# Performance work log

Hardware: AMD Instinct MI355X
Metric: run time of the kernel (lower is better)

## Reference

```python
import jax, jax.numpy as jnp
import numpy as np

B, LA, LS, C, H = 4, 1536, 512, 256, 4
DK = C // H
NEG = -jnp.inf


def _pad(lengths, maxlen):
    # True where padded (idx >= length)
    return jnp.arange(maxlen)[None, :] >= lengths[:, None]


def build_mask(l_v, l_s, ilens, ylens):
    """Additive float mask [B, l_v+l_s, l_v+l_s] with 0 / -inf, matching
    generate_multi_modal_mask_new."""
    b = ilens.shape[0]
    i = jnp.arange(l_s)
    causal = jnp.where(i[:, None] >= i[None, :], 0.0, NEG)            # [l_s, l_s]
    tgt_pad = _pad(ylens, l_s)                                        # [b, l_s]
    mask_s_s = jnp.where(tgt_pad[:, None, :], NEG, causal[None])      # [b, l_s, l_s]
    src_row = jnp.where(_pad(ilens, l_v), NEG, 0.0)                   # [b, l_v]
    mask_v_v = jnp.broadcast_to(src_row[:, None, :], (b, l_v, l_v))
    mask_s_v = jnp.broadcast_to(src_row[:, None, :], (b, l_s, l_v))
    mask_v_s = jnp.full((b, l_v, l_s), NEG, dtype=jnp.float32)
    top = jnp.concatenate([mask_v_v, mask_v_s], axis=2)
    bot = jnp.concatenate([mask_s_v, mask_s_s], axis=2)
    return jnp.concatenate([top, bot], axis=1)


def setup_inputs() -> dict:
    key = jax.random.key(0)
    ks = jax.random.split(key, 12)
    scale = 1.0 / np.sqrt(C)
    return {
        "audio_encoder_out": jax.random.normal(ks[0], (B, LA, C), jnp.float32),
        "text_encoder_out": jax.random.normal(ks[1], (B, LS, C), jnp.float32),
        "speech_length": jax.random.randint(ks[2], (B,), 1, LA),
        "text_length": jax.random.randint(ks[3], (B,), 1, LS),
        "Wq": jax.random.normal(ks[4], (C, C), jnp.float32) * scale,
        "bq": jax.random.normal(ks[5], (C,), jnp.float32) * scale,
        "Wk": jax.random.normal(ks[6], (C, C), jnp.float32) * scale,
        "bk": jax.random.normal(ks[7], (C,), jnp.float32) * scale,
        "Wv": jax.random.normal(ks[8], (C, C), jnp.float32) * scale,
        "bv": jax.random.normal(ks[9], (C,), jnp.float32) * scale,
        "Wo": jax.random.normal(ks[10], (C, C), jnp.float32) * scale,
        "bo": jax.random.normal(ks[11], (C,), jnp.float32) * scale,
    }


def reference(audio_encoder_out, text_encoder_out, speech_length, text_length,
              Wq, bq, Wk, bk, Wv, bv, Wo, bo):
    b, l_a, c = audio_encoder_out.shape
    l_s = text_encoder_out.shape[1]
    x = jnp.concatenate([audio_encoder_out, text_encoder_out], axis=1)  # [B, L, C]
    L = l_a + l_s

    def heads(W, bias):
        return (x @ W.T + bias).reshape(b, L, H, DK).transpose(0, 2, 1, 3)  # [B,H,L,DK]

    q, k, v = heads(Wq, bq), heads(Wk, bk), heads(Wv, bv)
    scores = jnp.einsum("bhqd,bhkd->bhqk", q, k) / np.float32(np.sqrt(DK))

    amask = build_mask(l_a, l_s, speech_length, text_length)  # additive [B,L,L]
    # Faithful to torch: mask.eq(0) positions (additive-0) are filled with -inf,
    # then zeroed in attn (the module's inverted masking behavior).
    eq0 = (amask == 0.0)[:, None, :, :]                       # [B,1,L,L]
    scores = jnp.where(eq0, NEG, scores)
    attn = jax.nn.softmax(scores, axis=-1)
    attn = jnp.where(eq0, 0.0, attn)                          # (dropout = identity, eval)
    out = jnp.einsum("bhqk,bhkd->bhqd", attn, v)
    out = out.transpose(0, 2, 1, 3).reshape(b, L, H * DK)
    return out @ Wo.T + bo
```

## Files before the change

### kernel.cpp

```cpp
#include <hip/hip_runtime.h>
#include <hip/hip_bf16.h>
#include <math.h>

#define LA 1536
#define LS 512
#define LT 2048
#define CC 256
#define NH 4
#define DKH 64
#define NB 4
#define NT (LT / 64)
#define NTA (LA / 64)

typedef _Float16 f16;
typedef __attribute__((ext_vector_type(8))) _Float16 f16x8;
typedef __attribute__((ext_vector_type(4))) _Float16 f16x4;
typedef __attribute__((ext_vector_type(4))) float f32x4;

__device__ inline f16x8 cvt8(const float4 a, const float4 b) {
    f16x8 h;
    h[0] = (_Float16)a.x; h[1] = (_Float16)a.y; h[2] = (_Float16)a.z; h[3] = (_Float16)a.w;
    h[4] = (_Float16)b.x; h[5] = (_Float16)b.y; h[6] = (_Float16)b.z; h[7] = (_Float16)b.w;
    return h;
}

__global__ __launch_bounds__(256) void qkv_mfma(
    const float* __restrict__ audio, const float* __restrict__ text,
    const float* __restrict__ Wq, const float* __restrict__ bq,
    const float* __restrict__ Wk, const float* __restrict__ bk,
    const float* __restrict__ Wv, const float* __restrict__ bv,
    f16* __restrict__ Qh, f16* __restrict__ Kh, f16* __restrict__ Vth)
{
    __shared__ f16 smem[128 * 64 + 64 * 64];
    f16* As = smem;
    f16* Bs = smem + 128 * 64;

    const int tid = threadIdx.x;
    const int w = tid >> 6, l = tid & 63;
    const int g = l >> 4, r = l & 15;

    const int m0 = blockIdx.x * 128;
    const int n0 = blockIdx.y * 64;
    const int mat = n0 >> 8;
    const int ch0 = n0 & 255;

    const float* W    = (mat == 0) ? Wq : (mat == 1) ? Wk : Wv;
    const float* bias = (mat == 0) ? bq : (mat == 1) ? bk : bv;

    const int b  = m0 >> 11;
    const int l0 = m0 & 2047;

    f32x4 acc[2][4] = {};

    for (int k0 = 0; k0 < CC; k0 += 64) {
        #pragma unroll
        for (int m = 0; m < 4; ++m) {
            const int idx = m * 256 + tid;
            const int row = idx >> 3, c = idx & 7;
            const int lrow = l0 + row;
            const float* src = (lrow < LA)
                ? (audio + ((size_t)b * LA + lrow) * CC + k0 + c * 8)
                : (text  + ((size_t)b * LS + (lrow - LA)) * CC + k0 + c * 8);
            const float4 x0 = *(const float4*)src;
            const float4 x1 = *(const float4*)(src + 4);
            *(f16x8*)(As + row * 64 + ((c ^ (row & 7)) << 3)) = cvt8(x0, x1);
        }
        #pragma unroll
        for (int m = 0; m < 2; ++m) {
            const int idx = m * 256 + tid;
            const int row = idx >> 3, c = idx & 7;
            const float* src = W + (size_t)(ch0 + row) * CC + k0 + c * 8;
            const float4 x0 = *(const float4*)src;
            const float4 x1 = *(const float4*)(src + 4);
            *(f16x8*)(Bs + row * 64 + ((c ^ (row & 7)) << 3)) = cvt8(x0, x1);
        }
        __syncthreads();
        #pragma unroll
        for (int kc = 0; kc < 2; ++kc) {
            f16x8 af[2];
            #pragma unroll
            for (int i = 0; i < 2; ++i) {
                const int row = w * 32 + i * 16 + r;
                const int c = kc * 4 + g;
                af[i] = *(const f16x8*)(As + row * 64 + ((c ^ (row & 7)) << 3));
            }
            f16x8 bf[4];
            #pragma unroll
            for (int j = 0; j < 4; ++j) {
                const int row = j * 16 + r;
                const int c = kc * 4 + g;
                bf[j] = *(const f16x8*)(Bs + row * 64 + ((c ^ (row & 7)) << 3));
            }
            #pragma unroll
            for (int i = 0; i < 2; ++i)
                #pragma unroll
                for (int j = 0; j < 4; ++j)
                    acc[i][j] = __builtin_amdgcn_mfma_f32_16x16x32_f16(af[i], bf[j], acc[i][j], 0, 0, 0);
        }
        __syncthreads();
    }

    float bcol[4];
    #pragma unroll
    for (int j = 0; j < 4; ++j) bcol[j] = bias[ch0 + j * 16 + r];

    if (mat <= 1) {
        f16* Out = (mat == 0) ? Qh : Kh;
        #pragma unroll
        for (int i = 0; i < 2; ++i)
            #pragma unroll
            for (int e = 0; e < 4; ++e) {
                const int m = m0 + w * 32 + i * 16 + g * 4 + e;
                #pragma unroll
                for (int j = 0; j < 4; ++j)
                    Out[(size_t)m * CC + ch0 + j * 16 + r] = (_Float16)(acc[i][j][e] + bcol[j]);
            }
    } else {
        f16* Ts = smem;
        #pragma unroll
        for (int i = 0; i < 2; ++i)
            #pragma unroll
            for (int e = 0; e < 4; ++e) {
                const int ml = w * 32 + i * 16 + g * 4 + e;
                #pragma unroll
                for (int j = 0; j < 4; ++j)
                    Ts[(j * 16 + r) * 136 + ml] = (_Float16)(acc[i][j][e] + bcol[j]);
            }
        __syncthreads();
        const int b2 = m0 >> 11, l0m = m0 & 2047;
        #pragma unroll
        for (int u = 0; u < 4; ++u) {
            const int idx = u * 256 + tid;
            const int nl = idx >> 4, mc = idx & 15;
            const f16x8 vv = *(const f16x8*)(Ts + nl * 136 + mc * 8);
            const int nglob = ch0 + nl;
            const int hh = nglob >> 6, dd = nglob & 63;
            *(f16x8*)(Vth + ((size_t)((b2 * NH + hh) * DKH + dd)) * LT + l0m + mc * 8) = vv;
        }
    }
}

__global__ __launch_bounds__(512) void attn_f16(
    const f16* __restrict__ Q, const f16* __restrict__ K,
    const f16* __restrict__ Vt,
    const int* __restrict__ slen, const int* __restrict__ tlen,
    f16* __restrict__ AO)
{
    __shared__ f16 Ks[2][4096];
    __shared__ f16 Vts[2][4096];
    __shared__ f16 Ps[8][16 * 72];
    __shared__ float Oc[4][1024];
    __shared__ float ML[2][64][2];

    const int tid = threadIdx.x;
    const int w = tid >> 6, l = tid & 63;
    const int gid = w >> 2, wg = w & 3;
    const int g = l >> 4, r = l & 15;
    const int tg = tid & 255;

    const int q0 = blockIdx.x * 64;
    const int h  = blockIdx.y;
    const int b  = blockIdx.z;

    const int ilen = slen[b];
    const int kcap = LA + tlen[b];
    const int nskip = ilen >> 6;
    int ntskip = 0;
    if (q0 >= LA) {
        const int skipmax = min(q0 - 63, kcap - 64);
        const int d = skipmax - LA;
        ntskip = (d < 0) ? 0 : ((d >> 6) + 1);
    }
    const int nAudio = NTA - nskip;
    const int nProc  = nAudio + (NT - NTA) - ntskip;
    const int nIter  = (nProc + 1) >> 1;

    const int qrow = q0 + 16 * wg + r;

    f16x8 qf[2];
    #pragma unroll
    for (int ch = 0; ch < 2; ++ch) {
        f16x8 q8 = *(const f16x8*)(Q + ((size_t)(b * LT) + qrow) * CC + h * DKH + ch * 32 + g * 8);
        #pragma unroll
        for (int e = 0; e < 8; ++e) q8[e] = q8[e] * (_Float16)0.125f;
        qf[ch] = q8;
    }

    const int srow0 = tg >> 3, scc = tg & 7;
    const int srow1 = srow0 + 32;
    const int sdst0 = srow0 * 64 + ((scc ^ (srow0 & 7)) << 3);
    const int sdst1 = srow1 * 64 + ((scc ^ (srow1 & 7)) << 3);

    #define TILE_OF(p) ((p) < nAudio ? (nskip + (p)) : (NTA + ntskip + ((p) - nAudio)))

    {
        const int k0 = TILE_OF(gid) * 64;
        *(f16x8*)(Ks[gid] + sdst0)  = *(const f16x8*)(K  + ((size_t)(b * LT) + k0 + srow0) * CC + h * DKH + scc * 8);
        *(f16x8*)(Vts[gid] + sdst0) = *(const f16x8*)(Vt + ((size_t)((b * NH + h) * DKH) + srow0) * LT + k0 + scc * 8);
        *(f16x8*)(Ks[gid] + sdst1)  = *(const f16x8*)(K  + ((size_t)(b * LT) + k0 + srow1) * CC + h * DKH + scc * 8);
        *(f16x8*)(Vts[gid] + sdst1) = *(const f16x8*)(Vt + ((size_t)((b * NH + h) * DKH) + srow1) * LT + k0 + scc * 8);
    }

    float m_run = -1e30f, l_run = 0.0f;
    f32x4 o[4] = {};

    for (int i = 0; i < nIter; ++i) {
        __syncthreads();
        const int pcur = 2 * i + gid;
        const bool curV = pcur < nProc;
        const bool nxtV = (pcur + 2) < nProc;

        f16x8 kr0, vr0, kr1, vr1;
        if (nxtV) {
            const int kn = TILE_OF(pcur + 2) * 64;
            kr0 = *(const f16x8*)(K  + ((size_t)(b * LT) + kn + srow0) * CC + h * DKH + scc * 8);
            vr0 = *(const f16x8*)(Vt + ((size_t)((b * NH + h) * DKH) + srow0) * LT + kn + scc * 8);
            kr1 = *(const f16x8*)(K  + ((size_t)(b * LT) + kn + srow1) * CC + h * DKH + scc * 8);
            vr1 = *(const f16x8*)(Vt + ((size_t)((b * NH + h) * DKH) + srow1) * LT + kn + scc * 8);
        }

        if (curV) {
            const int kt = TILE_OF(pcur);
            const int k0 = kt * 64;

            f32x4 sacc[4] = {};
            #pragma unroll
            for (int s = 0; s < 4; ++s) {
                const int row = 16 * s + r;
                #pragma unroll
                for (int ch = 0; ch < 2; ++ch) {
                    const f16x8 a = *(const f16x8*)(Ks[gid] + row * 64 + ((((ch * 4 + g) ^ (row & 7)) & 7) << 3));
                    sacc[s] = __builtin_amdgcn_mfma_f32_16x16x32_f16(a, qf[ch], sacc[s], 0, 0, 0);
                }
            }

            const int mode = (kt < NTA) ? ((k0 >= ilen) ? 0 : 1)
                                        : ((q0 < LA) ? 0 : 2);
            float sv[16];
            if (mode == 0) {
                #pragma unroll
                for (int s = 0; s < 4; ++s)
                    #pragma unroll
                    for (int e = 0; e < 4; ++e) sv[s * 4 + e] = sacc[s][e];
            } else if (mode == 1) {
                #pragma unroll
                for (int s = 0; s < 4; ++s)
                    #pragma unroll
                    for (int e = 0; e < 4; ++e) {
                        const int kk = k0 + 16 * s + 4 * g + e;
                        sv[s * 4 + e] = (kk >= ilen) ? sacc[s][e] : -INFINITY;
                    }
            } else {
                #pragma unroll
                for (int s = 0; s < 4; ++s)
                    #pragma unroll
                    for (int e = 0; e < 4; ++e) {
                        const int kk = k0 + 16 * s + 4 * g + e;
                        sv[s * 4 + e] = (kk > qrow || kk >= kcap) ? sacc[s][e] : -INFINITY;
                    }
            }

            float mloc = -1e30f;
            #pragma unroll
            for (int u = 0; u < 16; ++u) mloc = fmaxf(mloc, sv[u]);
            mloc = fmaxf(mloc, __shfl_xor(mloc, 16));
            mloc = fmaxf(mloc, __shfl_xor(mloc, 32));
            const float m_new = fmaxf(m_run, mloc);

            float ssum = 0.0f;
            f16x4 ph[4];
            #pragma unroll
            for (int s = 0; s < 4; ++s)
                #pragma unroll
                for (int e = 0; e < 4; ++e) {
                    const float p = __expf(sv[s * 4 + e] - m_new);
                    ph[s][e] = (_Float16)p;
                    ssum += p;
                }
            ssum += __shfl_xor(ssum, 16);
            ssum += __shfl_xor(ssum, 32);
            const float sc = __expf(m_run - m_new);
            l_run = l_run * sc + ssum;
            m_run = m_new;

            #pragma unroll
            for (int s = 0; s < 4; ++s)
                *(f16x4*)(&Ps[w][0] + r * 72 + 16 * s + 4 * g) = ph[s];

            #pragma unroll
            for (int e = 0; e < 4; ++e) {
                const float scr = __shfl(sc, 4 * g + e);
                #pragma unroll
                for (int dsb = 0; dsb < 4; ++dsb) o[dsb][e] *= scr;
            }

            #pragma unroll
            for (int ch = 0; ch < 2; ++ch) {
                const f16x8 a = *(const f16x8*)(&Ps[w][0] + r * 72 + ch * 32 + g * 8);
                #pragma unroll
                for (int dsb = 0; dsb < 4; ++dsb) {
                    const int vrow = 16 * dsb + r;
                    const f16x8 bf = *(const f16x8*)(Vts[gid] + vrow * 64 + ((((ch * 4 + g) ^ (vrow & 7)) & 7) << 3));
                    o[dsb] = __builtin_amdgcn_mfma_f32_16x16x32_f16(a, bf, o[dsb], 0, 0, 0);
                }
            }
        }

        __syncthreads();
        if (nxtV) {
            *(f16x8*)(Ks[gid] + sdst0)  = kr0;
            *(f16x8*)(Vts[gid] + sdst0) = vr0;
            *(f16x8*)(Ks[gid] + sdst1)  = kr1;
            *(f16x8*)(Vts[gid] + sdst1) = vr1;
        }
    }

    if (g == 0) {
        ML[gid][16 * wg + r][0] = m_run;
        ML[gid][16 * wg + r][1] = l_run;
    }
    if (gid == 1) {
        #pragma unroll
        for (int dsb = 0; dsb < 4; ++dsb)
            *(f32x4*)&Oc[wg][dsb * 256 + (g * 16 + r) * 4] = o[dsb];
    }
    __syncthreads();

    if (gid == 0) {
        #pragma unroll
        for (int e = 0; e < 4; ++e) {
            const int qloc = 16 * wg + 4 * g + e;
            const float m0v = ML[0][qloc][0], l0v = ML[0][qloc][1];
            const float m1v = ML[1][qloc][0], l1v = ML[1][qloc][1];
            const float mt = fmaxf(m0v, m1v);
            const float c0 = __expf(m0v - mt);
            const float c1 = __expf(m1v - mt);
            const float inv = 1.0f / (l0v * c0 + l1v * c1);
            const int qq = q0 + qloc;
            #pragma unroll
            for (int dsb = 0; dsb < 4; ++dsb) {
                const float of = (o[dsb][e] * c0 + Oc[wg][dsb * 256 + (g * 16 + r) * 4 + e] * c1) * inv;
                AO[((size_t)(b * LT) + qq) * CC + h * DKH + 16 * dsb + r] = (_Float16)of;
            }
        }
    }
    #undef TILE_OF
}

__global__ __launch_bounds__(256) void out_mfma(
    const f16* __restrict__ X, const float* __restrict__ Wo,
    const float* __restrict__ bo, float* __restrict__ Out)
{
    __shared__ f16 As[128 * 64];
    __shared__ f16 Bs[64 * 64];

    const int tid = threadIdx.x;
    const int w = tid >> 6, l = tid & 63;
    const int g = l >> 4, r = l & 15;

    const int m0 = blockIdx.x * 128;
    const int n0 = blockIdx.y * 64;

    f32x4 acc[2][4] = {};

    for (int k0 = 0; k0 < CC; k0 += 64) {
        #pragma unroll
        for (int m = 0; m < 4; ++m) {
            const int idx = m * 256 + tid;
            const int row = idx >> 3, c = idx & 7;
            *(f16x8*)(As + row * 64 + ((c ^ (row & 7)) << 3)) =
                *(const f16x8*)(X + (size_t)(m0 + row) * CC + k0 + c * 8);
        }
        #pragma unroll
        for (int m = 0; m < 2; ++m) {
            const int idx = m * 256 + tid;
            const int row = idx >> 3, c = idx & 7;
            const float* src = Wo + (size_t)(n0 + row) * CC + k0 + c * 8;
            const float4 x0 = *(const float4*)src;
            const float4 x1 = *(const float4*)(src + 4);
            *(f16x8*)(Bs + row * 64 + ((c ^ (row & 7)) << 3)) = cvt8(x0, x1);
        }
        __syncthreads();
        #pragma unroll
        for (int kc = 0; kc < 2; ++kc) {
            f16x8 af[2];
            #pragma unroll
            for (int i = 0; i < 2; ++i) {
                const int row = w * 32 + i * 16 + r;
                const int c = kc * 4 + g;
                af[i] = *(const f16x8*)(As + row * 64 + ((c ^ (row & 7)) << 3));
            }
            f16x8 bf[4];
            #pragma unroll
            for (int j = 0; j < 4; ++j) {
                const int row = j * 16 + r;
                const int c = kc * 4 + g;
                bf[j] = *(const f16x8*)(Bs + row * 64 + ((c ^ (row & 7)) << 3));
            }
            #pragma unroll
            for (int i = 0; i < 2; ++i)
                #pragma unroll
                for (int j = 0; j < 4; ++j)
                    acc[i][j] = __builtin_amdgcn_mfma_f32_16x16x32_f16(af[i], bf[j], acc[i][j], 0, 0, 0);
        }
        __syncthreads();
    }

    float bcol[4];
    #pragma unroll
    for (int j = 0; j < 4; ++j) bcol[j] = bo[n0 + j * 16 + r];

    #pragma unroll
    for (int i = 0; i < 2; ++i)
        #pragma unroll
        for (int e = 0; e < 4; ++e) {
            const int m = m0 + w * 32 + i * 16 + g * 4 + e;
            #pragma unroll
            for (int j = 0; j < 4; ++j)
                Out[(size_t)m * CC + n0 + j * 16 + r] = acc[i][j][e] + bcol[j];
        }
}

extern "C" void kernel_launch(void* const* d_in, const int* in_sizes, int n_in,
                              void* d_out, int out_size, void* d_ws, size_t ws_size,
                              hipStream_t stream)
{
    const float* audio = (const float*)d_in[0];
    const float* text  = (const float*)d_in[1];
    const int*   slen  = (const int*)d_in[2];
    const int*   tlen  = (const int*)d_in[3];
    const float* Wq = (const float*)d_in[4];
    const float* bq = (const float*)d_in[5];
    const float* Wk = (const float*)d_in[6];
    const float* bk = (const float*)d_in[7];
    const float* Wv = (const float*)d_in[8];
    const float* bv = (const float*)d_in[9];
    const float* Wo = (const float*)d_in[10];
    const float* bo = (const float*)d_in[11];
    float* out = (float*)d_out;

    const size_t SZ = (size_t)NB * LT * CC;
    f16* Qh  = (f16*)d_ws;
    f16* Kh  = Qh + SZ;
    f16* Vth = Kh + SZ;
    f16* AOh = Vth + SZ;

    qkv_mfma<<<dim3(64, 12), 256, 0, stream>>>(audio, text, Wq, bq, Wk, bk, Wv, bv,
                                               Qh, Kh, Vth);
    attn_f16<<<dim3(LT / 64, NH, NB), 512, 0, stream>>>(Qh, Kh, Vth, slen, tlen, AOh);
    out_mfma<<<dim3(64, 4), 256, 0, stream>>>(AOh, Wo, bo, out);
}
```

Baseline: 49.30 us.

## Split attention KV range four ways with combine kernel, widen GEMM tiles

Attention now uses a flash-decoding style split: each block handles every fourth KV tile and writes normalized partial outputs plus per-row max/sum, and a new combine kernel merges them. The aim is more blocks in flight and shorter per-block loops. The Q scale and log2(e) are folded into the QKV epilogue so the softmax can use exp2f, and rescaling of the running output is skipped when the running max is unchanged. The QKV and output GEMMs move to 128-wide N tiles, giving fewer blocks with more reuse. This adds a kernel launch and extra workspace traffic for the partial outputs.

```diff
diff --git a/kernel.cpp b/kernel.cpp
--- a/kernel.cpp
+++ b/kernel.cpp
@@ -11,6 +11,10 @@
 #define NB 4
 #define NT (LT / 64)
 #define NTA (LA / 64)
+#define NSPLIT 4
+#define SZ ((size_t)NB * LT * CC)
+
+#define QSCALE 0.1803368801111244f
 
 typedef _Float16 f16;
 typedef __attribute__((ext_vector_type(8))) _Float16 f16x8;
@@ -31,7 +35,7 @@
     const float* __restrict__ Wv, const float* __restrict__ bv,
     f16* __restrict__ Qh, f16* __restrict__ Kh, f16* __restrict__ Vth)
 {
-    __shared__ f16 smem[128 * 64 + 64 * 64];
+    __shared__ f16 smem[128 * 64 + 128 * 64];
     f16* As = smem;
     f16* Bs = smem + 128 * 64;
 
@@ -40,9 +44,9 @@
     const int g = l >> 4, r = l & 15;
 
     const int m0 = blockIdx.x * 128;
-    const int n0 = blockIdx.y * 64;
-    const int mat = n0 >> 8;
-    const int ch0 = n0 & 255;
+    const int n0g = blockIdx.y * 128;
+    const int mat = n0g >> 8;
+    const int ch0 = n0g & 255;
 
     const float* W    = (mat == 0) ? Wq : (mat == 1) ? Wk : Wv;
     const float* bias = (mat == 0) ? bq : (mat == 1) ? bk : bv;
@@ -50,12 +54,12 @@
     const int b  = m0 >> 11;
     const int l0 = m0 & 2047;
 
-    f32x4 acc[2][4] = {};
+    f32x4 acc[2][8] = {};
 
     for (int k0 = 0; k0 < CC; k0 += 64) {
         #pragma unroll
-        for (int m = 0; m < 4; ++m) {
-            const int idx = m * 256 + tid;
+        for (int mm = 0; mm < 4; ++mm) {
+            const int idx = mm * 256 + tid;
             const int row = idx >> 3, c = idx & 7;
             const int lrow = l0 + row;
             const float* src = (lrow < LA)
@@ -66,8 +70,8 @@
             *(f16x8*)(As + row * 64 + ((c ^ (row & 7)) << 3)) = cvt8(x0, x1);
         }
         #pragma unroll
-        for (int m = 0; m < 2; ++m) {
-            const int idx = m * 256 + tid;
+        for (int mm = 0; mm < 4; ++mm) {
+            const int idx = mm * 256 + tid;
             const int row = idx >> 3, c = idx & 7;
             const float* src = W + (size_t)(ch0 + row) * CC + k0 + c * 8;
             const float4 x0 = *(const float4*)src;
@@ -84,83 +88,91 @@
                 const int c = kc * 4 + g;
                 af[i] = *(const f16x8*)(As + row * 64 + ((c ^ (row & 7)) << 3));
             }
-            f16x8 bf[4];
-            #pragma unroll
-            for (int j = 0; j < 4; ++j) {
-                const int row = j * 16 + r;
-                const int c = kc * 4 + g;
-                bf[j] = *(const f16x8*)(Bs + row * 64 + ((c ^ (row & 7)) << 3));
-            }
-            #pragma unroll
-            for (int i = 0; i < 2; ++i)
-                #pragma unroll
-                for (int j = 0; j < 4; ++j)
-                    acc[i][j] = __builtin_amdgcn_mfma_f32_16x16x32_f16(af[i], bf[j], acc[i][j], 0, 0, 0);
-        }
-        __syncthreads();
-    }
-
-    float bcol[4];
-    #pragma unroll
-    for (int j = 0; j < 4; ++j) bcol[j] = bias[ch0 + j * 16 + r];
+            #pragma unroll
+            for (int jh = 0; jh < 2; ++jh) {
+                f16x8 bf[4];
+                #pragma unroll
+                for (int j = 0; j < 4; ++j) {
+                    const int row = (jh * 4 + j) * 16 + r;
+                    const int c = kc * 4 + g;
+                    bf[j] = *(const f16x8*)(Bs + row * 64 + ((c ^ (row & 7)) << 3));
+                }
+                #pragma unroll
+                for (int i = 0; i < 2; ++i)
+                    #pragma unroll
+                    for (int j = 0; j < 4; ++j)
+                        acc[i][jh * 4 + j] = __builtin_amdgcn_mfma_f32_16x16x32_f16(
+                            af[i], bf[j], acc[i][jh * 4 + j], 0, 0, 0);
+            }
+        }
+        __syncthreads();
+    }
+
+    float bcol[8];
+    #pragma unroll
+    for (int j = 0; j < 8; ++j) bcol[j] = bias[ch0 + j * 16 + r];
 
     if (mat <= 1) {
         f16* Out = (mat == 0) ? Qh : Kh;
+        const float osc = (mat == 0) ? QSCALE : 1.0f;
         #pragma unroll
         for (int i = 0; i < 2; ++i)
             #pragma unroll
             for (int e = 0; e < 4; ++e) {
                 const int m = m0 + w * 32 + i * 16 + g * 4 + e;
                 #pragma unroll
-                for (int j = 0; j < 4; ++j)
-                    Out[(size_t)m * CC + ch0 + j * 16 + r] = (_Float16)(acc[i][j][e] + bcol[j]);
+                for (int j = 0; j < 8; ++j)
+                    Out[(size_t)m * CC + ch0 + j * 16 + r] =
+                        (_Float16)((acc[i][j][e] + bcol[j]) * osc);
             }
     } else {
         f16* Ts = smem;
-        #pragma unroll
-        for (int i = 0; i < 2; ++i)
-            #pragma unroll
-            for (int e = 0; e < 4; ++e) {
-                const int ml = w * 32 + i * 16 + g * 4 + e;
-                #pragma unroll
-                for (int j = 0; j < 4; ++j)
-                    Ts[(j * 16 + r) * 136 + ml] = (_Float16)(acc[i][j][e] + bcol[j]);
-            }
-        __syncthreads();
         const int b2 = m0 >> 11, l0m = m0 & 2047;
         #pragma unroll
-        for (int u = 0; u < 4; ++u) {
-            const int idx = u * 256 + tid;
-            const int nl = idx >> 4, mc = idx & 15;
-            const f16x8 vv = *(const f16x8*)(Ts + nl * 136 + mc * 8);
-            const int nglob = ch0 + nl;
-            const int hh = nglob >> 6, dd = nglob & 63;
-            *(f16x8*)(Vth + ((size_t)((b2 * NH + hh) * DKH + dd)) * LT + l0m + mc * 8) = vv;
-        }
-    }
-}
-
-__global__ __launch_bounds__(512) void attn_f16(
+        for (int pass = 0; pass < 2; ++pass) {
+            #pragma unroll
+            for (int i = 0; i < 2; ++i)
+                #pragma unroll
+                for (int e = 0; e < 4; ++e) {
+                    const int ml = w * 32 + i * 16 + g * 4 + e;
+                    #pragma unroll
+                    for (int j = 0; j < 4; ++j)
+                        Ts[(j * 16 + r) * 136 + ml] =
+                            (_Float16)(acc[i][pass * 4 + j][e] + bcol[pass * 4 + j]);
+                }
+            __syncthreads();
+            #pragma unroll
+            for (int u = 0; u < 4; ++u) {
+                const int idx = u * 256 + tid;
+                const int nl = idx >> 4, mc = idx & 15;
+                const f16x8 vv = *(const f16x8*)(Ts + nl * 136 + mc * 8);
+                const int nglob = ch0 + pass * 64 + nl;
+                const int hh = nglob >> 6, dd = nglob & 63;
+                *(f16x8*)(Vth + ((size_t)((b2 * NH + hh) * DKH + dd)) * LT + l0m + mc * 8) = vv;
+            }
+            __syncthreads();
+        }
+    }
+}
+
+__global__ __launch_bounds__(256) void attn_f16(
     const f16* __restrict__ Q, const f16* __restrict__ K,
     const f16* __restrict__ Vt,
     const int* __restrict__ slen, const int* __restrict__ tlen,
-    f16* __restrict__ AO)
+    f16* __restrict__ Po, float2* __restrict__ Ml)
 {
-    __shared__ f16 Ks[2][4096];
-    __shared__ f16 Vts[2][4096];
-    __shared__ f16 Ps[8][16 * 72];
-    __shared__ float Oc[4][1024];
-    __shared__ float ML[2][64][2];
+    __shared__ f16 Ks[4096];
+    __shared__ f16 Vts[4096];
+    __shared__ f16 Ps[4][16 * 72];
 
     const int tid = threadIdx.x;
     const int w = tid >> 6, l = tid & 63;
-    const int gid = w >> 2, wg = w & 3;
     const int g = l >> 4, r = l & 15;
-    const int tg = tid & 255;
 
     const int q0 = blockIdx.x * 64;
     const int h  = blockIdx.y;
-    const int b  = blockIdx.z;
+    const int b  = blockIdx.z >> 2;
+    const int sp = blockIdx.z & 3;
 
     const int ilen = slen[b];
     const int kcap = LA + tlen[b];
@@ -173,178 +185,199 @@
     }
     const int nAudio = NTA - nskip;
     const int nProc  = nAudio + (NT - NTA) - ntskip;
-    const int nIter  = (nProc + 1) >> 1;
-
-    const int qrow = q0 + 16 * wg + r;
+    const int nIter  = (nProc > sp) ? ((nProc - sp + NSPLIT - 1) >> 2) : 0;
+
+    const int qrow = q0 + 16 * w + r;
 
     f16x8 qf[2];
     #pragma unroll
-    for (int ch = 0; ch < 2; ++ch) {
-        f16x8 q8 = *(const f16x8*)(Q + ((size_t)(b * LT) + qrow) * CC + h * DKH + ch * 32 + g * 8);
-        #pragma unroll
-        for (int e = 0; e < 8; ++e) q8[e] = q8[e] * (_Float16)0.125f;
-        qf[ch] = q8;
-    }
-
-    const int srow0 = tg >> 3, scc = tg & 7;
+    for (int ch = 0; ch < 2; ++ch)
+        qf[ch] = *(const f16x8*)(Q + ((size_t)(b * LT) + qrow) * CC + h * DKH + ch * 32 + g * 8);
+
+    const int srow0 = tid >> 3, scc = tid & 7;
     const int srow1 = srow0 + 32;
     const int sdst0 = srow0 * 64 + ((scc ^ (srow0 & 7)) << 3);
     const int sdst1 = srow1 * 64 + ((scc ^ (srow1 & 7)) << 3);
 
     #define TILE_OF(p) ((p) < nAudio ? (nskip + (p)) : (NTA + ntskip + ((p) - nAudio)))
 
-    {
-        const int k0 = TILE_OF(gid) * 64;
-        *(f16x8*)(Ks[gid] + sdst0)  = *(const f16x8*)(K  + ((size_t)(b * LT) + k0 + srow0) * CC + h * DKH + scc * 8);
-        *(f16x8*)(Vts[gid] + sdst0) = *(const f16x8*)(Vt + ((size_t)((b * NH + h) * DKH) + srow0) * LT + k0 + scc * 8);
-        *(f16x8*)(Ks[gid] + sdst1)  = *(const f16x8*)(K  + ((size_t)(b * LT) + k0 + srow1) * CC + h * DKH + scc * 8);
-        *(f16x8*)(Vts[gid] + sdst1) = *(const f16x8*)(Vt + ((size_t)((b * NH + h) * DKH) + srow1) * LT + k0 + scc * 8);
-    }
+    if (nIter > 0) {
+        const int k0 = TILE_OF(sp) * 64;
+        *(f16x8*)(Ks + sdst0)  = *(const f16x8*)(K  + ((size_t)(b * LT) + k0 + srow0) * CC + h * DKH + scc * 8);
+        *(f16x8*)(Vts + sdst0) = *(const f16x8*)(Vt + ((size_t)((b * NH + h) * DKH) + srow0) * LT + k0 + scc * 8);
+        *(f16x8*)(Ks + sdst1)  = *(const f16x8*)(K  + ((size_t)(b * LT) + k0 + srow1) * CC + h * DKH + scc * 8);
+        *(f16x8*)(Vts + sdst1) = *(const f16x8*)(Vt + ((size_t)((b * NH + h) * DKH) + srow1) * LT + k0 + scc * 8);
+    }
+    __syncthreads();
 
     float m_run = -1e30f, l_run = 0.0f;
     f32x4 o[4] = {};
 
     for (int i = 0; i < nIter; ++i) {
-        __syncthreads();
-        const int pcur = 2 * i + gid;
-        const bool curV = pcur < nProc;
-        const bool nxtV = (pcur + 2) < nProc;
+        const int pcur = sp + NSPLIT * i;
+        const int kt = TILE_OF(pcur);
+        const int k0 = kt * 64;
+        const bool nxtV = (pcur + NSPLIT) < nProc;
 
         f16x8 kr0, vr0, kr1, vr1;
         if (nxtV) {
-            const int kn = TILE_OF(pcur + 2) * 64;
+            const int kn = TILE_OF(pcur + NSPLIT) * 64;
             kr0 = *(const f16x8*)(K  + ((size_t)(b * LT) + kn + srow0) * CC + h * DKH + scc * 8);
             vr0 = *(const f16x8*)(Vt + ((size_t)((b * NH + h) * DKH) + srow0) * LT + kn + scc * 8);
             kr1 = *(const f16x8*)(K  + ((size_t)(b * LT) + kn + srow1) * CC + h * DKH + scc * 8);
             vr1 = *(const f16x8*)(Vt + ((size_t)((b * NH + h) * DKH) + srow1) * LT + kn + scc * 8);
         }
 
-        if (curV) {
-            const int kt = TILE_OF(pcur);
-            const int k0 = kt * 64;
-
-            f32x4 sacc[4] = {};
-            #pragma unroll
-            for (int s = 0; s < 4; ++s) {
-                const int row = 16 * s + r;
-                #pragma unroll
-                for (int ch = 0; ch < 2; ++ch) {
-                    const f16x8 a = *(const f16x8*)(Ks[gid] + row * 64 + ((((ch * 4 + g) ^ (row & 7)) & 7) << 3));
-                    sacc[s] = __builtin_amdgcn_mfma_f32_16x16x32_f16(a, qf[ch], sacc[s], 0, 0, 0);
+        f32x4 sacc[4] = {};
+        #pragma unroll
+        for (int s = 0; s < 4; ++s) {
+            const int row = 16 * s + r;
+            #pragma unroll
+            for (int ch = 0; ch < 2; ++ch) {
+                const f16x8 a = *(const f16x8*)(Ks + row * 64 + ((((ch * 4 + g) ^ (row & 7)) & 7) << 3));
+                sacc[s] = __builtin_amdgcn_mfma_f32_16x16x32_f16(a, qf[ch], sacc[s], 0, 0, 0);
+            }
+        }
+
+        const int mode = (kt < NTA) ? ((k0 >= ilen) ? 0 : 1)
+                                    : ((q0 < LA) ? 0 : 2);
+        float sv[16];
+        if (mode == 0) {
+            #pragma unroll
+            for (int s = 0; s < 4; ++s)
+                #pragma unroll
+                for (int e = 0; e < 4; ++e) sv[s * 4 + e] = sacc[s][e];
+        } else if (mode == 1) {
+            #pragma unroll
+            for (int s = 0; s < 4; ++s)
+                #pragma unroll
+                for (int e = 0; e < 4; ++e) {
+                    const int kk = k0 + 16 * s + 4 * g + e;
+                    sv[s * 4 + e] = (kk >= ilen) ? sacc[s][e] : -INFINITY;
                 }
-            }
-
-            const int mode = (kt < NTA) ? ((k0 >= ilen) ? 0 : 1)
-                                        : ((q0 < LA) ? 0 : 2);
-            float sv[16];
-            if (mode == 0) {
-                #pragma unroll
-                for (int s = 0; s < 4; ++s)
-                    #pragma unroll
-                    for (int e = 0; e < 4; ++e) sv[s * 4 + e] = sacc[s][e];
-            } else if (mode == 1) {
-                #pragma unroll
-                for (int s = 0; s < 4; ++s)
-                    #pragma unroll
-                    for (int e = 0; e < 4; ++e) {
-                        const int kk = k0 + 16 * s + 4 * g + e;
-                        sv[s * 4 + e] = (kk >= ilen) ? sacc[s][e] : -INFINITY;
-                    }
-            } else {
-                #pragma unroll
-                for (int s = 0; s < 4; ++s)
-                    #pragma unroll
-                    for (int e = 0; e < 4; ++e) {
-                        const int kk = k0 + 16 * s + 4 * g + e;
-                        sv[s * 4 + e] = (kk > qrow || kk >= kcap) ? sacc[s][e] : -INFINITY;
-                    }
-            }
-
-            float mloc = -1e30f;
-            #pragma unroll
-            for (int u = 0; u < 16; ++u) mloc = fmaxf(mloc, sv[u]);
-            mloc = fmaxf(mloc, __shfl_xor(mloc, 16));
-            mloc = fmaxf(mloc, __shfl_xor(mloc, 32));
-            const float m_new = fmaxf(m_run, mloc);
-
-            float ssum = 0.0f;
-            f16x4 ph[4];
+        } else {
             #pragma unroll
             for (int s = 0; s < 4; ++s)
                 #pragma unroll
                 for (int e = 0; e < 4; ++e) {
-                    const float p = __expf(sv[s * 4 + e] - m_new);
-                    ph[s][e] = (_Float16)p;
-                    ssum += p;
+                    const int kk = k0 + 16 * s + 4 * g + e;
+                    sv[s * 4 + e] = (kk > qrow || kk >= kcap) ? sacc[s][e] : -INFINITY;
                 }
-            ssum += __shfl_xor(ssum, 16);
-            ssum += __shfl_xor(ssum, 32);
-            const float sc = __expf(m_run - m_new);
+        }
+
+        float mloc = -1e30f;
+        #pragma unroll
+        for (int u = 0; u < 16; ++u) mloc = fmaxf(mloc, sv[u]);
+        mloc = fmaxf(mloc, __shfl_xor(mloc, 16));
+        mloc = fmaxf(mloc, __shfl_xor(mloc, 32));
+        const float m_new = fmaxf(m_run, mloc);
+
+        float ssum = 0.0f;
+        f16x4 ph[4];
+        #pragma unroll
+        for (int s = 0; s < 4; ++s)
+            #pragma unroll
+            for (int e = 0; e < 4; ++e) {
+                const float p = exp2f(sv[s * 4 + e] - m_new);
+                ph[s][e] = (_Float16)p;
+                ssum += p;
+            }
+        ssum += __shfl_xor(ssum, 16);
+        ssum += __shfl_xor(ssum, 32);
+
+        if (__all(m_new == m_run)) {
+            l_run += ssum;
+        } else {
+            const float sc = exp2f(m_run - m_new);
             l_run = l_run * sc + ssum;
             m_run = m_new;
-
-            #pragma unroll
-            for (int s = 0; s < 4; ++s)
-                *(f16x4*)(&Ps[w][0] + r * 72 + 16 * s + 4 * g) = ph[s];
-
             #pragma unroll
             for (int e = 0; e < 4; ++e) {
                 const float scr = __shfl(sc, 4 * g + e);
                 #pragma unroll
                 for (int dsb = 0; dsb < 4; ++dsb) o[dsb][e] *= scr;
             }
-
-            #pragma unroll
-            for (int ch = 0; ch < 2; ++ch) {
-                const f16x8 a = *(const f16x8*)(&Ps[w][0] + r * 72 + ch * 32 + g * 8);
-                #pragma unroll
-                for (int dsb = 0; dsb < 4; ++dsb) {
-                    const int vrow = 16 * dsb + r;
-                    const f16x8 bf = *(const f16x8*)(Vts[gid] + vrow * 64 + ((((ch * 4 + g) ^ (vrow & 7)) & 7) << 3));
-                    o[dsb] = __builtin_amdgcn_mfma_f32_16x16x32_f16(a, bf, o[dsb], 0, 0, 0);
-                }
+        }
+
+        #pragma unroll
+        for (int s = 0; s < 4; ++s)
+            *(f16x4*)(&Ps[w][0] + r * 72 + 16 * s + 4 * g) = ph[s];
+
+        #pragma unroll
+        for (int ch = 0; ch < 2; ++ch) {
+            const f16x8 a = *(const f16x8*)(&Ps[w][0] + r * 72 + ch * 32 + g * 8);
+            #pragma unroll
+            for (int dsb = 0; dsb < 4; ++dsb) {
+                const int vrow = 16 * dsb + r;
+                const f16x8 bf = *(const f16x8*)(Vts + vrow * 64 + ((((ch * 4 + g) ^ (vrow & 7)) & 7) << 3));
+                o[dsb] = __builtin_amdgcn_mfma_f32_16x16x32_f16(a, bf, o[dsb], 0, 0, 0);
             }
         }
 
         __syncthreads();
         if (nxtV) {
-            *(f16x8*)(Ks[gid] + sdst0)  = kr0;
-            *(f16x8*)(Vts[gid] + sdst0) = vr0;
-            *(f16x8*)(Ks[gid] + sdst1)  = kr1;
-            *(f16x8*)(Vts[gid] + sdst1) = vr1;
-        }
-    }
-
-    if (g == 0) {
-        ML[gid][16 * wg + r][0] = m_run;
-        ML[gid][16 * wg + r][1] = l_run;
-    }
-    if (gid == 1) {
+            *(f16x8*)(Ks + sdst0)  = kr0;
+            *(f16x8*)(Vts + sdst0) = vr0;
+            *(f16x8*)(Ks + sdst1)  = kr1;
+            *(f16x8*)(Vts + sdst1) = vr1;
+        }
+        __syncthreads();
+    }
+
+    const float linv = (l_run > 0.0f) ? 1.0f / l_run : 0.0f;
+    #pragma unroll
+    for (int e = 0; e < 4; ++e) {
+        const float inv = __shfl(linv, 4 * g + e);
+        const int qq = q0 + 16 * w + 4 * g + e;
         #pragma unroll
         for (int dsb = 0; dsb < 4; ++dsb)
-            *(f32x4*)&Oc[wg][dsb * 256 + (g * 16 + r) * 4] = o[dsb];
-    }
-    __syncthreads();
-
-    if (gid == 0) {
-        #pragma unroll
-        for (int e = 0; e < 4; ++e) {
-            const int qloc = 16 * wg + 4 * g + e;
-            const float m0v = ML[0][qloc][0], l0v = ML[0][qloc][1];
-            const float m1v = ML[1][qloc][0], l1v = ML[1][qloc][1];
-            const float mt = fmaxf(m0v, m1v);
-            const float c0 = __expf(m0v - mt);
-            const float c1 = __expf(m1v - mt);
-            const float inv = 1.0f / (l0v * c0 + l1v * c1);
-            const int qq = q0 + qloc;
-            #pragma unroll
-            for (int dsb = 0; dsb < 4; ++dsb) {
-                const float of = (o[dsb][e] * c0 + Oc[wg][dsb * 256 + (g * 16 + r) * 4 + e] * c1) * inv;
-                AO[((size_t)(b * LT) + qq) * CC + h * DKH + 16 * dsb + r] = (_Float16)of;
-            }
-        }
-    }
+            Po[(size_t)sp * SZ + ((size_t)(b * LT) + qq) * CC + h * DKH + 16 * dsb + r] =
+                (_Float16)(o[dsb][e] * inv);
+    }
+    if (g == 0)
+        Ml[((size_t)(sp * NB + b) * NH + h) * LT + q0 + 16 * w + r] =
+            make_float2(m_run, l_run);
     #undef TILE_OF
+}
+
+__global__ __launch_bounds__(256) void attn_combine(
+    const f16* __restrict__ Po, const float2* __restrict__ Ml,
+    f16* __restrict__ AOh)
+{
+    const int idx = blockIdx.x * 256 + threadIdx.x;
+    const size_t flat = (size_t)idx * 8;
+    const int qg = (int)(flat >> 8);
+    const int c  = (int)(flat & 255);
+    const int b  = qg >> 11, q = qg & 2047;
+    const int h  = c >> 6;
+
+    float m_i[NSPLIT], l_i[NSPLIT];
+    float mt = -1e30f;
+    #pragma unroll
+    for (int s = 0; s < NSPLIT; ++s) {
+        const float2 ml = Ml[((size_t)(s * NB + b) * NH + h) * LT + q];
+        m_i[s] = ml.x; l_i[s] = ml.y;
+        mt = fmaxf(mt, m_i[s]);
+    }
+    float wgt[NSPLIT], denom = 0.0f;
+    #pragma unroll
+    for (int s = 0; s < NSPLIT; ++s) {
+        wgt[s] = l_i[s] * exp2f(m_i[s] - mt);
+        denom += wgt[s];
+    }
+    const float inv = 1.0f / denom;
+
+    float a8[8] = {};
+    #pragma unroll
+    for (int s = 0; s < NSPLIT; ++s) {
+        const f16x8 o8 = *(const f16x8*)(Po + (size_t)s * SZ + flat);
+        #pragma unroll
+        for (int e = 0; e < 8; ++e) a8[e] += wgt[s] * (float)o8[e];
+    }
+    f16x8 r8;
+    #pragma unroll
+    for (int e = 0; e < 8; ++e) r8[e] = (_Float16)(a8[e] * inv);
+    *(f16x8*)(AOh + flat) = r8;
 }
 
 __global__ __launch_bounds__(256) void out_mfma(
@@ -352,28 +385,28 @@
     const float* __restrict__ bo, float* __restrict__ Out)
 {
     __shared__ f16 As[128 * 64];
-    __shared__ f16 Bs[64 * 64];
+    __shared__ f16 Bs[128 * 64];
 
     const int tid = threadIdx.x;
     const int w = tid >> 6, l = tid & 63;
     const int g = l >> 4, r = l & 15;
 
     const int m0 = blockIdx.x * 128;
-    const int n0 = blockIdx.y * 64;
-
-    f32x4 acc[2][4] = {};
+    const int n0 = blockIdx.y * 128;
+
+    f32x4 acc[2][8] = {};
 
     for (int k0 = 0; k0 < CC; k0 += 64) {
         #pragma unroll
-        for (int m = 0; m < 4; ++m) {
-            const int idx = m * 256 + tid;
+        for (int mm = 0; mm < 4; ++mm) {
+            const int idx = mm * 256 + tid;
             const int row = idx >> 3, c = idx & 7;
             *(f16x8*)(As + row * 64 + ((c ^ (row & 7)) << 3)) =
                 *(const f16x8*)(X + (size_t)(m0 + row) * CC + k0 + c * 8);
         }
         #pragma unroll
-        for (int m = 0; m < 2; ++m) {
-            const int idx = m * 256 + tid;
+        for (int mm = 0; mm < 4; ++mm) {
+            const int idx = mm * 256 + tid;
             const int row = idx >> 3, c = idx & 7;
             const float* src = Wo + (size_t)(n0 + row) * CC + k0 + c * 8;
             const float4 x0 = *(const float4*)src;
@@ -390,25 +423,29 @@
                 const int c = kc * 4 + g;
                 af[i] = *(const f16x8*)(As + row * 64 + ((c ^ (row & 7)) << 3));
             }
-            f16x8 bf[4];
-            #pragma unroll
-            for (int j = 0; j < 4; ++j) {
-                const int row = j * 16 + r;
-                const int c = kc * 4 + g;
-                bf[j] = *(const f16x8*)(Bs + row * 64 + ((c ^ (row & 7)) << 3));
-            }
-            #pragma unroll
-            for (int i = 0; i < 2; ++i)
-                #pragma unroll
-                for (int j = 0; j < 4; ++j)
-                    acc[i][j] = __builtin_amdgcn_mfma_f32_16x16x32_f16(af[i], bf[j], acc[i][j], 0, 0, 0);
-        }
-        __syncthreads();
-    }
-
-    float bcol[4];
-    #pragma unroll
-    for (int j = 0; j < 4; ++j) bcol[j] = bo[n0 + j * 16 + r];
+            #pragma unroll
+            for (int jh = 0; jh < 2; ++jh) {
+                f16x8 bf[4];
+                #pragma unroll
+                for (int j = 0; j < 4; ++j) {
+                    const int row = (jh * 4 + j) * 16 + r;
+                    const int c = kc * 4 + g;
+                    bf[j] = *(const f16x8*)(Bs + row * 64 + ((c ^ (row & 7)) << 3));
+                }
+                #pragma unroll
+                for (int i = 0; i < 2; ++i)
+                    #pragma unroll
+                    for (int j = 0; j < 4; ++j)
+                        acc[i][jh * 4 + j] = __builtin_amdgcn_mfma_f32_16x16x32_f16(
+                            af[i], bf[j], acc[i][jh * 4 + j], 0, 0, 0);
+            }
+        }
+        __syncthreads();
+    }
+
+    float bcol[8];
+    #pragma unroll
+    for (int j = 0; j < 8; ++j) bcol[j] = bo[n0 + j * 16 + r];
 
     #pragma unroll
     for (int i = 0; i < 2; ++i)
@@ -416,7 +453,7 @@
         for (int e = 0; e < 4; ++e) {
             const int m = m0 + w * 32 + i * 16 + g * 4 + e;
             #pragma unroll
-            for (int j = 0; j < 4; ++j)
+            for (int j = 0; j < 8; ++j)
                 Out[(size_t)m * CC + n0 + j * 16 + r] = acc[i][j][e] + bcol[j];
         }
 }
@@ -439,14 +476,17 @@
     const float* bo = (const float*)d_in[11];
     float* out = (float*)d_out;
 
-    const size_t SZ = (size_t)NB * LT * CC;
     f16* Qh  = (f16*)d_ws;
     f16* Kh  = Qh + SZ;
     f16* Vth = Kh + SZ;
     f16* AOh = Vth + SZ;
-
-    qkv_mfma<<<dim3(64, 12), 256, 0, stream>>>(audio, text, Wq, bq, Wk, bk, Wv, bv,
-                                               Qh, Kh, Vth);
-    attn_f16<<<dim3(LT / 64, NH, NB), 512, 0, stream>>>(Qh, Kh, Vth, slen, tlen, AOh);
-    out_mfma<<<dim3(64, 4), 256, 0, stream>>>(AOh, Wo, bo, out);
-}
+    f16* Po  = AOh + SZ;
+    float2* Ml = (float2*)(Po + (size_t)NSPLIT * SZ);
+
+    qkv_mfma<<<dim3(64, 6), 256, 0, stream>>>(audio, text, Wq, bq, Wk, bk, Wv, bv,
+                                              Qh, Kh, Vth);
+    attn_f16<<<dim3(LT / 64, NH, NB * NSPLIT), 256, 0, stream>>>(Qh, Kh, Vth,
+                                                                 slen, tlen, Po, Ml);
+    attn_combine<<<dim3((NB * LT * CC / 8) / 256), 256, 0, stream>>>(Po, Ml, AOh);
+    out_mfma<<<dim3(64, 2), 256, 0, stream>>>(AOh, Wo, bo, out);
+}
```

Result: slower. 59.43 us (+20.5%).
